# Kernel optimization log

Measured on AMD Instinct MI355X. Metric: run time of the kernel, lower is better.

The kernel has to match this reference:

```python
import jax, jax.numpy as jnp
import numpy as np

NUM_CLASSES = 91
W_CLASS, W_BBOX, W_GIOU = 1.0, 5.0, 2.0


def cxcywh_to_xyxy(b):
    return jnp.concatenate([b[..., :2] - 0.5 * b[..., 2:], b[..., :2] + 0.5 * b[..., 2:]], axis=-1)


def pairwise_giou(b1, b2):
    # b1: [B,Q,4] xyxy, b2: [B,G,4] xyxy -> [B,Q,G]
    area1 = (b1[..., 2] - b1[..., 0]) * (b1[..., 3] - b1[..., 1])
    area2 = (b2[..., 2] - b2[..., 0]) * (b2[..., 3] - b2[..., 1])
    lt = jnp.maximum(b1[:, :, None, :2], b2[:, None, :, :2])
    rb = jnp.minimum(b1[:, :, None, 2:], b2[:, None, :, 2:])
    wh = jnp.clip(rb - lt, 0.0)
    inter = wh[..., 0] * wh[..., 1]
    union = area1[:, :, None] + area2[:, None, :] - inter
    iou = inter / union
    lt2 = jnp.minimum(b1[:, :, None, :2], b2[:, None, :, :2])
    rb2 = jnp.maximum(b1[:, :, None, 2:], b2[:, None, :, 2:])
    wh2 = jnp.clip(rb2 - lt2, 0.0)
    area_c = wh2[..., 0] * wh2[..., 1]
    return iou - (area_c - union) / area_c


def elem_giou(b1, b2):
    # b1, b2: [M,4] xyxy -> [M]
    area1 = (b1[:, 2] - b1[:, 0]) * (b1[:, 3] - b1[:, 1])
    area2 = (b2[:, 2] - b2[:, 0]) * (b2[:, 3] - b2[:, 1])
    lt = jnp.maximum(b1[:, :2], b2[:, :2])
    rb = jnp.minimum(b1[:, 2:], b2[:, 2:])
    wh = jnp.clip(rb - lt, 0.0)
    inter = wh[:, 0] * wh[:, 1]
    union = area1 + area2 - inter
    iou = inter / union
    lt2 = jnp.minimum(b1[:, :2], b2[:, :2])
    rb2 = jnp.maximum(b1[:, 2:], b2[:, 2:])
    wh2 = jnp.clip(rb2 - lt2, 0.0)
    area_c = wh2[:, 0] * wh2[:, 1]
    return iou - (area_c - union) / area_c


def _lsa(cost):
    # Rectangular linear sum assignment (scipy-style shortest augmenting path).
    cost = np.asarray(cost, dtype=np.float64)
    transposed = cost.shape[0] > cost.shape[1]
    if transposed:
        cost = cost.T
    n, m = cost.shape
    u = np.zeros(n)
    v = np.zeros(m)
    path = np.full(m, -1, dtype=np.int64)
    col4row = np.full(n, -1, dtype=np.int64)
    row4col = np.full(m, -1, dtype=np.int64)
    for cur_row in range(n):
        min_val = 0.0
        i = cur_row
        remaining = np.arange(m)
        SR = np.zeros(n, dtype=bool)
        SC = np.zeros(m, dtype=bool)
        shortest = np.full(m, np.inf)
        sink = -1
        while sink == -1:
            SR[i] = True
            r = min_val + cost[i, remaining] - u[i] - v[remaining]
            better = r < shortest[remaining]
            upd = remaining[better]
            shortest[upd] = r[better]
            path[upd] = i
            k = int(np.argmin(shortest[remaining]))
            j = int(remaining[k])
            min_val = shortest[j]
            if not np.isfinite(min_val):
                raise ValueError('infeasible cost matrix')
            if row4col[j] == -1:
                sink = j
            else:
                i = int(row4col[j])
            SC[j] = True
            remaining = np.delete(remaining, k)
        u[cur_row] += min_val
        sr = SR.copy()
        sr[cur_row] = False
        u[sr] += min_val - shortest[col4row[sr]]
        v[SC] -= min_val - shortest[SC]
        j = sink
        while True:
            i = int(path[j])
            row4col[j] = i
            col4row[i], j = j, col4row[i]
            if i == cur_row:
                break
    if transposed:
        a = np.argsort(col4row)
        return col4row[a], a
    return np.arange(n), col4row


def _match(pred_logits, pred_boxes, gt_labels, gt_boxes):
    B, Q, _ = pred_logits.shape
    G = gt_labels.shape[1]
    log_probs = jax.nn.log_softmax(pred_logits, axis=-1)  # [B,Q,C+1]
    labels_c = jnp.clip(gt_labels, 0, NUM_CLASSES)
    cost_class = -jnp.take_along_axis(log_probs, jnp.broadcast_to(labels_c[:, None, :], (B, Q, G)), axis=2)
    cost_bbox = jnp.sum(jnp.abs(pred_boxes[:, :, None, :] - gt_boxes[:, None, :, :]), axis=-1)  # pairwise L1
    cost_giou = -pairwise_giou(cxcywh_to_xyxy(pred_boxes), cxcywh_to_xyxy(gt_boxes))
    C = W_BBOX * cost_bbox + W_CLASS * cost_class + W_GIOU * cost_giou  # [B,Q,G]
    C_np = np.asarray(jax.lax.stop_gradient(C))
    valid = np.asarray(gt_labels) < NUM_CLASSES
    b_idx, s_idx, t_idx = [], [], []
    for i in range(B):  # Hungarian is inherently sequential / host-side (matches torch original)
        cols = np.nonzero(valid[i])[0]
        if cols.size == 0:
            continue
        r, c = _lsa(C_np[i][:, cols])
        b_idx.append(np.full(r.shape, i, dtype=np.int64))
        s_idx.append(r.astype(np.int64))
        t_idx.append(cols[c].astype(np.int64))
    return np.concatenate(b_idx), np.concatenate(s_idx), np.concatenate(t_idx)


def _losses(pred_logits, pred_boxes, gt_boxes, gt_labels, batch_idx, src_idx, tgt_idx):
    B, Q, _ = pred_logits.shape
    log_probs = jax.nn.log_softmax(pred_logits, axis=-1)
    target_classes = jnp.full((B, Q), NUM_CLASSES, dtype=jnp.int32)
    target_classes = target_classes.at[batch_idx, src_idx].set(gt_labels[batch_idx, tgt_idx].astype(jnp.int32))
    nll = -jnp.take_along_axis(log_probs, target_classes[..., None], axis=-1)[..., 0]  # [B,Q]
    empty_weight = jnp.concatenate([jnp.full((NUM_CLASSES,), 0.1, jnp.float32), jnp.ones((1,), jnp.float32)])
    w = empty_weight[target_classes]
    loss_ce = jnp.sum(w * nll) / jnp.sum(w)  # weighted CE, torch 'mean' semantics
    mp = pred_boxes[batch_idx, src_idx][..., :4]
    mg = gt_boxes[batch_idx, tgt_idx]
    loss_bbox = jnp.mean(jnp.abs(mp - mg))
    loss_giou = jnp.mean(1.0 - elem_giou(cxcywh_to_xyxy(mp), cxcywh_to_xyxy(mg)))
    return jnp.stack([loss_ce, loss_bbox, loss_giou])


def setup_inputs() -> dict:
    key = jax.random.key(0)
    k1, k2, k3, k4 = jax.random.split(key, 4)
    B, Q, G = 128, 900, 80
    return {
        'pred_logits': jax.random.normal(k1, (B, Q, NUM_CLASSES + 1), dtype=jnp.float32),
        'pred_boxes': jax.random.uniform(k2, (B, Q, 4), dtype=jnp.float32),
        'gt_labels': jax.random.randint(k3, (B, G), 0, 120, dtype=jnp.int32),
        'gt_boxes': jax.random.uniform(k4, (B, G, 4), dtype=jnp.float32),
    }


def reference(pred_logits, pred_boxes, gt_labels, gt_boxes):
    bi, si, ti = _match(pred_logits, pred_boxes, gt_labels, gt_boxes)
    return _losses(pred_logits, pred_boxes, gt_boxes, gt_labels, bi, si, ti)
```

## Files before the change

### kernel.cpp

```cpp
#include <hip/hip_runtime.h>
#include <math.h>

#define BB 128
#define QQ 900
#define GG 80
#define CC 92
#define NCL 91
#define NSLOT 16

#define NPART 8
#define QPB 128

#define COST_OFF 0
#define LSE_OFF  36864000
#define VIDX_OFF 37324800
#define NV_OFF   37365760
#define FPART_OFF 37366272
#define MPART_OFF 37370368

#define FRONT_LDS_BYTES (QPB * 93 * 4)

__global__ __launch_bounds__(128) void front_kernel(const float* __restrict__ logits,
                                                    const float* __restrict__ pboxes,
                                                    const float* __restrict__ gboxes,
                                                    const int* __restrict__ glabels,
                                                    float* __restrict__ lse_g,
                                                    int* __restrict__ valid_idx,
                                                    int* __restrict__ nvalid,
                                                    float* __restrict__ cost,
                                                    float* __restrict__ fpart) {
    extern __shared__ float sL[];
    __shared__ int svidx[GG];
    __shared__ int s_n;
    __shared__ int slab[GG];
    __shared__ float sgx0[GG], sgy0[GG], sgx1[GG], sgy1[GG], sgar[GG];
    __shared__ float sgcx[GG], sgcy[GG], sgcz[GG], sgcw[GG];
    __shared__ double sce[2];
    int blk = blockIdx.x;
    int b = blk >> 3;
    int part = blk & 7;
    int tid = threadIdx.x;
    int q0 = part * QPB;
    int qcnt = QQ - q0;
    if (qcnt > QPB) qcnt = QPB;
    if (tid < 64) {
        int lane = tid;
        bool v0 = glabels[b * GG + lane] < NCL;
        bool v1 = (lane < GG - 64) ? (glabels[b * GG + 64 + lane] < NCL) : false;
        unsigned long long m0 = __ballot(v0);
        unsigned long long m1 = __ballot(v1);
        int c0 = __popcll(m0);
        unsigned long long lower = lane ? (~0ULL >> (64 - lane)) : 0ULL;
        if (v0) { int p = __popcll(m0 & lower); svidx[p] = lane; valid_idx[b * GG + p] = lane; }
        if (v1) { int p = c0 + __popcll(m1 & lower); svidx[p] = 64 + lane; valid_idx[b * GG + p] = 64 + lane; }
        if (lane == 0) { s_n = c0 + __popcll(m1); nvalid[b] = s_n; }
    }
    __syncthreads();
    int n = s_n;

    {
        const float* src = logits + ((size_t)b * QQ + q0) * CC;
        for (int i = tid; i < qcnt * CC; i += 128) {
            int ql = i / CC;
            int c = i - ql * CC;
            sL[ql * 93 + c] = src[i];
        }
    }
    for (int k = tid; k < n; k += 128) {
        int g = svidx[k];
        slab[k] = glabels[b * GG + g];
        float4 gb = ((const float4*)gboxes)[b * GG + g];
        sgcx[k] = gb.x; sgcy[k] = gb.y; sgcz[k] = gb.z; sgcw[k] = gb.w;
        float gx0 = gb.x - 0.5f * gb.z, gy0 = gb.y - 0.5f * gb.w;
        float gx1 = gb.x + 0.5f * gb.z, gy1 = gb.y + 0.5f * gb.w;
        sgx0[k] = gx0; sgy0[k] = gy0; sgx1[k] = gx1; sgy1[k] = gy1;
        sgar[k] = (gx1 - gx0) * (gy1 - gy0);
    }
    __syncthreads();

    int q = q0 + tid;
    bool qok = tid < qcnt;
    const float* row = sL + tid * 93;

    double local = 0.0;
    float lse_q = 0.f;
    if (qok) {
        float mx = -INFINITY;
        for (int c = 0; c < 23; ++c) {
            float x0 = row[4 * c], x1 = row[4 * c + 1], x2 = row[4 * c + 2], x3 = row[4 * c + 3];
            mx = fmaxf(mx, fmaxf(fmaxf(x0, x1), fmaxf(x2, x3)));
        }
        float ssum = 0.f;
        float e91 = 0.f;
        for (int c = 0; c < 23; ++c) {
            float x0 = row[4 * c], x1 = row[4 * c + 1], x2 = row[4 * c + 2], x3 = row[4 * c + 3];
            ssum += expf(x0 - mx) + expf(x1 - mx) + expf(x2 - mx) + expf(x3 - mx);
            if (c == 22) e91 = x3;
        }
        lse_q = mx + logf(ssum);
        lse_g[b * QQ + q] = lse_q;
        local = (double)lse_q - (double)e91;
    }
#pragma unroll
    for (int off = 32; off; off >>= 1) local += __shfl_down(local, off);
    if ((tid & 63) == 0) sce[tid >> 6] = local;

    if (qok) {
        float4 pb = ((const float4*)pboxes)[b * QQ + q];
        float px0 = pb.x - 0.5f * pb.z, py0 = pb.y - 0.5f * pb.w;
        float px1 = pb.x + 0.5f * pb.z, py1 = pb.y + 0.5f * pb.w;
        float parea = (px1 - px0) * (py1 - py0);
        for (int k = 0; k < n; ++k) {
            float l1 = fabsf(pb.x - sgcx[k]) + fabsf(pb.y - sgcy[k]) +
                       fabsf(pb.z - sgcz[k]) + fabsf(pb.w - sgcw[k]);
            float ltx = fmaxf(px0, sgx0[k]), lty = fmaxf(py0, sgy0[k]);
            float rbx = fminf(px1, sgx1[k]), rby = fminf(py1, sgy1[k]);
            float iw = fmaxf(rbx - ltx, 0.f), ih = fmaxf(rby - lty, 0.f);
            float inter = iw * ih;
            float uni = parea + sgar[k] - inter;
            float iou = inter / uni;
            float cx0 = fminf(px0, sgx0[k]), cy0 = fminf(py0, sgy0[k]);
            float cx1 = fmaxf(px1, sgx1[k]), cy1 = fmaxf(py1, sgy1[k]);
            float cw = fmaxf(cx1 - cx0, 0.f), ch = fmaxf(cy1 - cy0, 0.f);
            float ac = cw * ch;
            float giou = iou - (ac - uni) / ac;
            float cls = lse_q - row[slab[k]];
            cost[((size_t)(b * GG + k)) * QQ + q] = 5.f * l1 + cls - 2.f * giou;
        }
    }
    __syncthreads();
    if (tid == 0) fpart[blk] = (float)(sce[0] + sce[1]);
}

__device__ __forceinline__ unsigned long long wave_min_u64(unsigned long long x) {
#define KSTEP(ctrl)                                                                              \
    {                                                                                            \
        unsigned lo = (unsigned)x, hi = (unsigned)(x >> 32);                                     \
        unsigned lo_t = (unsigned)__builtin_amdgcn_update_dpp((int)lo, (int)lo, ctrl, 0xF, 0xF,  \
                                                              false);                            \
        unsigned hi_t = (unsigned)__builtin_amdgcn_update_dpp((int)hi, (int)hi, ctrl, 0xF, 0xF,  \
                                                              false);                            \
        unsigned long long t = ((unsigned long long)hi_t << 32) | lo_t;                          \
        x = t < x ? t : x;                                                                       \
    }
    KSTEP(0x111) KSTEP(0x112) KSTEP(0x114) KSTEP(0x118) KSTEP(0x142) KSTEP(0x143)
#undef KSTEP
    unsigned lo = (unsigned)__builtin_amdgcn_readlane((int)(unsigned)x, 63);
    unsigned hi = (unsigned)__builtin_amdgcn_readlane((int)(unsigned)(x >> 32), 63);
    return ((unsigned long long)hi << 32) | lo;
}

#define COL_OWNER_LANE(j) (((j) & 255) >> 2)
#define COL_SLOT(j) (((((j) >> 8)) << 2) | ((j) & 3))

__device__ __forceinline__ void load_row_f4(const float* crow, int lane, float (&cv)[NSLOT]) {
    const float4* c4 = (const float4*)crow;
    float4 a0 = c4[lane];
    float4 a1 = c4[64 + lane];
    float4 a2 = c4[128 + lane];
    float4 a3 = make_float4(0.f, 0.f, 0.f, 0.f);
    if (lane <= 32) a3 = c4[192 + lane];
    cv[0] = a0.x; cv[1] = a0.y; cv[2] = a0.z; cv[3] = a0.w;
    cv[4] = a1.x; cv[5] = a1.y; cv[6] = a1.z; cv[7] = a1.w;
    cv[8] = a2.x; cv[9] = a2.y; cv[10] = a2.z; cv[11] = a2.w;
    cv[12] = a3.x; cv[13] = a3.y; cv[14] = a3.z; cv[15] = a3.w;
}

__device__ __forceinline__ bool sap_phase(int cur, int lane, const float* cbase,
                                          unsigned valid_mask, float (&v)[NSLOT],
                                          int (&r4c_r)[NSLOT], float (&u_r)[2],
                                          int (&c4r_r)[2], float (&pf)[NSLOT], int nrows) {
    float sh[NSLOT];
    int path_r[NSLOT];
    float srv_r[2] = {0.f, 0.f};
    unsigned sc = 0, srm = 0;
#pragma unroll
    for (int s = 0; s < NSLOT; ++s) sh[s] = INFINITY;
    int i2 = cur;
    float minv = 0.f;
    int sink = -1;
    for (int pop = 0; pop < QQ && sink < 0; ++pop) {
        float cv[NSLOT];
        if (pop == 0) {
#pragma unroll
            for (int s = 0; s < NSLOT; ++s) cv[s] = pf[s];
        } else {
            load_row_f4(cbase + (size_t)i2 * QQ, lane, cv);
        }
        float uv = (i2 >> 6) ? u_r[1] : u_r[0];
        float ui = __uint_as_float(
            (unsigned)__builtin_amdgcn_readlane((int)__float_as_uint(uv), i2 & 63));
        float base = minv - ui;
        unsigned act = valid_mask & ~sc;
        float lmin = INFINITY;
        int lslot = 0;
#pragma unroll
        for (int s = 0; s < NSLOT; ++s) {
            if ((act >> s) & 1u) {
                float r = base + cv[s] - v[s];
                if (r < sh[s]) { sh[s] = r; path_r[s] = i2; }
                if (sh[s] < lmin) { lmin = sh[s]; lslot = s; }
            }
        }
        int jcol = ((lslot >> 2) << 8) + lane * 4 + (lslot & 3);
        unsigned u = __float_as_uint(lmin);
        u ^= ((int)u < 0) ? 0xFFFFFFFFu : 0x80000000u;
        unsigned long long key = ((unsigned long long)u << 32) | (unsigned)jcol;
        unsigned long long g = wave_min_u64(key);
        int lj = (int)(unsigned)g;
        unsigned mu = (unsigned)(g >> 32);
        minv = __uint_as_float((mu & 0x80000000u) ? (mu ^ 0x80000000u) : ~mu);
        int ol = COL_OWNER_LANE(lj);
        int os = COL_SLOT(lj);
        if (lane == ol) sc |= (1u << os);
        int rv = -1;
#pragma unroll
        for (int s = 0; s < NSLOT; ++s)
            if (s == os) rv = r4c_r[s];
        int r4c = __builtin_amdgcn_readlane(rv, ol);
        if (r4c == -1) {
            sink = lj;
        } else {
            i2 = r4c;
            if (lane == (i2 & 63)) {
#pragma unroll
                for (int s = 0; s < 2; ++s)
                    if (s == (i2 >> 6)) { srm |= (1u << s); srv_r[s] = minv; }
            }
        }
    }
    if (sink < 0) return false;
    {
        int nxt = cur + 2;
        if (nxt < nrows) load_row_f4(cbase + (size_t)nxt * QQ, lane, pf);
    }
    if (lane == (cur & 63)) {
#pragma unroll
        for (int s = 0; s < 2; ++s)
            if (s == (cur >> 6)) u_r[s] += minv;
    }
#pragma unroll
    for (int s = 0; s < 2; ++s)
        if ((srm >> s) & 1u) u_r[s] += minv - srv_r[s];
#pragma unroll
    for (int s = 0; s < NSLOT; ++s)
        if ((sc >> s) & 1u) v[s] -= (minv - sh[s]);
    int j = sink;
    while (true) {
        int plane = COL_OWNER_LANE(j);
        int pslot = COL_SLOT(j);
        int pv = 0;
#pragma unroll
        for (int s = 0; s < NSLOT; ++s)
            if (s == pslot) pv = path_r[s];
        int pi = __builtin_amdgcn_readlane(pv, plane);
        if (lane == plane) {
#pragma unroll
            for (int s = 0; s < NSLOT; ++s)
                if (s == pslot) r4c_r[s] = pi;
        }
        int cslot = pi >> 6, clane = pi & 63;
        int cvv = 0;
#pragma unroll
        for (int s = 0; s < 2; ++s)
            if (s == cslot) cvv = c4r_r[s];
        int nj = __builtin_amdgcn_readlane(cvv, clane);
        if (lane == clane) {
#pragma unroll
            for (int s = 0; s < 2; ++s)
                if (s == cslot) c4r_r[s] = j;
        }
        j = nj;
        if (pi == cur) break;
    }
    return true;
}

__global__ __launch_bounds__(64, 1) void lsa_kernel(const float* __restrict__ cost,
                                                    const int* __restrict__ nvalid,
                                                    const int* __restrict__ valid_idx,
                                                    const int* __restrict__ glabels,
                                                    const float* __restrict__ lse_g,
                                                    const float* __restrict__ pboxes,
                                                    const float* __restrict__ gboxes,
                                                    const float* __restrict__ logits,
                                                    double* __restrict__ mpart) {
    int b = blockIdx.x;
    int n = nvalid[b];
    const float* cbase = cost + (size_t)b * GG * QQ;
    int lane = threadIdx.x;

    float v[NSLOT];
    int r4c_r[NSLOT];
    float u_r[2];
    int c4r_r[2];
    float pfA[NSLOT], pfB[NSLOT];
    unsigned valid_mask = 0x0FFFu | ((lane <= 32) ? 0xF000u : 0u);
#pragma unroll
    for (int s = 0; s < NSLOT; ++s) { v[s] = 0.f; r4c_r[s] = -1; pfA[s] = 0.f; pfB[s] = 0.f; }
#pragma unroll
    for (int s = 0; s < 2; ++s) { u_r[s] = 0.f; c4r_r[s] = -1; }

    if (n > 0) load_row_f4(cbase, lane, pfA);
    if (n > 1) load_row_f4(cbase + QQ, lane, pfB);
    {
        int cur = 0;
        for (; cur + 1 < n; cur += 2) {
            sap_phase(cur, lane, cbase, valid_mask, v, r4c_r, u_r, c4r_r, pfA, n);
            sap_phase(cur + 1, lane, cbase, valid_mask, v, r4c_r, u_r, c4r_r, pfB, n);
        }
        if (cur < n)
            sap_phase(cur, lane, cbase, valid_mask, v, r4c_r, u_r, c4r_r, pfA, n);
    }

    double ce = 0.0, dl1 = 0.0, dgi = 0.0;
#pragma unroll
    for (int s = 0; s < 2; ++s) {
        int r = s * 64 + lane;
        int q = c4r_r[s];
        if (r < n && q >= 0 && q < QQ) {
            int g = valid_idx[b * GG + r];
            int label = glabels[b * GG + g];
            if (label < 0 || label >= CC) label = 0;
            size_t ro = ((size_t)b * QQ + q) * CC;
            float ls = lse_g[b * QQ + q];
            float nll_lab = ls - logits[ro + label];
            float nll_no = ls - logits[ro + NCL];
            ce += 0.1 * (double)nll_lab - (double)nll_no;
            float4 pb = ((const float4*)pboxes)[b * QQ + q];
            float4 gb = ((const float4*)gboxes)[b * GG + g];
            float l1 = fabsf(pb.x - gb.x) + fabsf(pb.y - gb.y) + fabsf(pb.z - gb.z) + fabsf(pb.w - gb.w);
            float px0 = pb.x - 0.5f * pb.z, py0 = pb.y - 0.5f * pb.w;
            float px1 = pb.x + 0.5f * pb.z, py1 = pb.y + 0.5f * pb.w;
            float gx0 = gb.x - 0.5f * gb.z, gy0 = gb.y - 0.5f * gb.w;
            float gx1 = gb.x + 0.5f * gb.z, gy1 = gb.y + 0.5f * gb.w;
            float parea = (px1 - px0) * (py1 - py0);
            float garea = (gx1 - gx0) * (gy1 - gy0);
            float ltx = fmaxf(px0, gx0), lty = fmaxf(py0, gy0);
            float rbx = fminf(px1, gx1), rby = fminf(py1, gy1);
            float iw = fmaxf(rbx - ltx, 0.f), ih = fmaxf(rby - lty, 0.f);
            float inter = iw * ih;
            float uni = parea + garea - inter;
            float iou = inter / uni;
            float cx0 = fminf(px0, gx0), cy0 = fminf(py0, gy0);
            float cx1 = fmaxf(px1, gx1), cy1 = fmaxf(py1, gy1);
            float cw = fmaxf(cx1 - cx0, 0.f), ch = fmaxf(cy1 - cy0, 0.f);
            float ac = cw * ch;
            float giou = iou - (ac - uni) / ac;
            dl1 += (double)l1;
            dgi += 1.0 - (double)giou;
        }
    }
#pragma unroll
    for (int off = 32; off; off >>= 1) {
        ce += __shfl_down(ce, off);
        dl1 += __shfl_down(dl1, off);
        dgi += __shfl_down(dgi, off);
    }
    if (lane == 0) {
        mpart[b * 3 + 0] = ce;
        mpart[b * 3 + 1] = dl1;
        mpart[b * 3 + 2] = dgi;
    }
}

__global__ __launch_bounds__(64) void final_kernel(const int* __restrict__ nvalid,
                                                   const float* __restrict__ fpart,
                                                   const double* __restrict__ mpart,
                                                   float* __restrict__ out) {
    int lane = threadIdx.x;
    int m = nvalid[lane] + nvalid[64 + lane];
    double fb = 0.0;
    for (int i = lane; i < BB * NPART; i += 64) fb += (double)fpart[i];
    double ce = 0.0, dl1 = 0.0, dgi = 0.0;
#pragma unroll
    for (int s = 0; s < 2; ++s) {
        int bb = s * 64 + lane;
        ce += mpart[bb * 3 + 0];
        dl1 += mpart[bb * 3 + 1];
        dgi += mpart[bb * 3 + 2];
    }
#pragma unroll
    for (int off = 32; off; off >>= 1) {
        m += __shfl_down(m, off);
        fb += __shfl_down(fb, off);
        ce += __shfl_down(ce, off);
        dl1 += __shfl_down(dl1, off);
        dgi += __shfl_down(dgi, off);
    }
    if (lane == 0) {
        double M = (double)m;
        double sum_w = (double)(BB * QQ) - 0.9 * M;
        out[0] = (float)((fb + ce) / sum_w);
        out[1] = (float)(dl1 / (4.0 * M));
        out[2] = (float)(dgi / M);
    }
}

extern "C" void kernel_launch(void* const* d_in, const int* in_sizes, int n_in,
                              void* d_out, int out_size, void* d_ws, size_t ws_size,
                              hipStream_t stream) {
    const float* logits = (const float*)d_in[0];
    const float* pboxes = (const float*)d_in[1];
    const int* glabels = (const int*)d_in[2];
    const float* gboxes = (const float*)d_in[3];
    float* out = (float*)d_out;

    char* ws = (char*)d_ws;
    float* cost = (float*)(ws + COST_OFF);
    float* lse = (float*)(ws + LSE_OFF);
    int* vidx = (int*)(ws + VIDX_OFF);
    int* nval = (int*)(ws + NV_OFF);
    float* fpart = (float*)(ws + FPART_OFF);
    double* mpart = (double*)(ws + MPART_OFF);

    (void)hipFuncSetAttribute((const void*)front_kernel,
                              hipFuncAttributeMaxDynamicSharedMemorySize, FRONT_LDS_BYTES);

    front_kernel<<<BB * NPART, 128, FRONT_LDS_BYTES, stream>>>(logits, pboxes, gboxes, glabels,
                                                               lse, vidx, nval, cost, fpart);
    lsa_kernel<<<BB, 64, 0, stream>>>(cost, nval, vidx, glabels, lse, pboxes, gboxes, logits, mpart);
    final_kernel<<<1, 64, 0, stream>>>(nval, fpart, mpart, out);
}
```

Measured before the change: 214.9 us.

## Fuse front, LSA and final kernels into one persistent launch with per-batch flags

Merges the three kernels into one grid. The first BB blocks run the assignment solver and spin on per-batch atomic counters until that batch's front blocks finish, and the last solver block to finish does the final reduction and resets the counters. The aim is to remove the launch gaps and let each batch's assignment start as soon as its cost matrix is ready, rather than waiting for every batch. In exchange, solver blocks now carry 128 threads and the front kernel's LDS allocation, and their spin-waiting depends on the front blocks being scheduled, which risks stalls or deadlock if residency is insufficient.

New measurement: 308.3 us. 1.43x slower.

```diff
diff --git a/kernel.cpp b/kernel.cpp
--- a/kernel.cpp
+++ b/kernel.cpp
@@ -20,117 +20,8 @@
 
 #define FRONT_LDS_BYTES (QPB * 93 * 4)
 
-__global__ __launch_bounds__(128) void front_kernel(const float* __restrict__ logits,
-                                                    const float* __restrict__ pboxes,
-                                                    const float* __restrict__ gboxes,
-                                                    const int* __restrict__ glabels,
-                                                    float* __restrict__ lse_g,
-                                                    int* __restrict__ valid_idx,
-                                                    int* __restrict__ nvalid,
-                                                    float* __restrict__ cost,
-                                                    float* __restrict__ fpart) {
-    extern __shared__ float sL[];
-    __shared__ int svidx[GG];
-    __shared__ int s_n;
-    __shared__ int slab[GG];
-    __shared__ float sgx0[GG], sgy0[GG], sgx1[GG], sgy1[GG], sgar[GG];
-    __shared__ float sgcx[GG], sgcy[GG], sgcz[GG], sgcw[GG];
-    __shared__ double sce[2];
-    int blk = blockIdx.x;
-    int b = blk >> 3;
-    int part = blk & 7;
-    int tid = threadIdx.x;
-    int q0 = part * QPB;
-    int qcnt = QQ - q0;
-    if (qcnt > QPB) qcnt = QPB;
-    if (tid < 64) {
-        int lane = tid;
-        bool v0 = glabels[b * GG + lane] < NCL;
-        bool v1 = (lane < GG - 64) ? (glabels[b * GG + 64 + lane] < NCL) : false;
-        unsigned long long m0 = __ballot(v0);
-        unsigned long long m1 = __ballot(v1);
-        int c0 = __popcll(m0);
-        unsigned long long lower = lane ? (~0ULL >> (64 - lane)) : 0ULL;
-        if (v0) { int p = __popcll(m0 & lower); svidx[p] = lane; valid_idx[b * GG + p] = lane; }
-        if (v1) { int p = c0 + __popcll(m1 & lower); svidx[p] = 64 + lane; valid_idx[b * GG + p] = 64 + lane; }
-        if (lane == 0) { s_n = c0 + __popcll(m1); nvalid[b] = s_n; }
-    }
-    __syncthreads();
-    int n = s_n;
-
-    {
-        const float* src = logits + ((size_t)b * QQ + q0) * CC;
-        for (int i = tid; i < qcnt * CC; i += 128) {
-            int ql = i / CC;
-            int c = i - ql * CC;
-            sL[ql * 93 + c] = src[i];
-        }
-    }
-    for (int k = tid; k < n; k += 128) {
-        int g = svidx[k];
-        slab[k] = glabels[b * GG + g];
-        float4 gb = ((const float4*)gboxes)[b * GG + g];
-        sgcx[k] = gb.x; sgcy[k] = gb.y; sgcz[k] = gb.z; sgcw[k] = gb.w;
-        float gx0 = gb.x - 0.5f * gb.z, gy0 = gb.y - 0.5f * gb.w;
-        float gx1 = gb.x + 0.5f * gb.z, gy1 = gb.y + 0.5f * gb.w;
-        sgx0[k] = gx0; sgy0[k] = gy0; sgx1[k] = gx1; sgy1[k] = gy1;
-        sgar[k] = (gx1 - gx0) * (gy1 - gy0);
-    }
-    __syncthreads();
-
-    int q = q0 + tid;
-    bool qok = tid < qcnt;
-    const float* row = sL + tid * 93;
-
-    double local = 0.0;
-    float lse_q = 0.f;
-    if (qok) {
-        float mx = -INFINITY;
-        for (int c = 0; c < 23; ++c) {
-            float x0 = row[4 * c], x1 = row[4 * c + 1], x2 = row[4 * c + 2], x3 = row[4 * c + 3];
-            mx = fmaxf(mx, fmaxf(fmaxf(x0, x1), fmaxf(x2, x3)));
-        }
-        float ssum = 0.f;
-        float e91 = 0.f;
-        for (int c = 0; c < 23; ++c) {
-            float x0 = row[4 * c], x1 = row[4 * c + 1], x2 = row[4 * c + 2], x3 = row[4 * c + 3];
-            ssum += expf(x0 - mx) + expf(x1 - mx) + expf(x2 - mx) + expf(x3 - mx);
-            if (c == 22) e91 = x3;
-        }
-        lse_q = mx + logf(ssum);
-        lse_g[b * QQ + q] = lse_q;
-        local = (double)lse_q - (double)e91;
-    }
-#pragma unroll
-    for (int off = 32; off; off >>= 1) local += __shfl_down(local, off);
-    if ((tid & 63) == 0) sce[tid >> 6] = local;
-
-    if (qok) {
-        float4 pb = ((const float4*)pboxes)[b * QQ + q];
-        float px0 = pb.x - 0.5f * pb.z, py0 = pb.y - 0.5f * pb.w;
-        float px1 = pb.x + 0.5f * pb.z, py1 = pb.y + 0.5f * pb.w;
-        float parea = (px1 - px0) * (py1 - py0);
-        for (int k = 0; k < n; ++k) {
-            float l1 = fabsf(pb.x - sgcx[k]) + fabsf(pb.y - sgcy[k]) +
-                       fabsf(pb.z - sgcz[k]) + fabsf(pb.w - sgcw[k]);
-            float ltx = fmaxf(px0, sgx0[k]), lty = fmaxf(py0, sgy0[k]);
-            float rbx = fminf(px1, sgx1[k]), rby = fminf(py1, sgy1[k]);
-            float iw = fmaxf(rbx - ltx, 0.f), ih = fmaxf(rby - lty, 0.f);
-            float inter = iw * ih;
-            float uni = parea + sgar[k] - inter;
-            float iou = inter / uni;
-            float cx0 = fminf(px0, sgx0[k]), cy0 = fminf(py0, sgy0[k]);
-            float cx1 = fmaxf(px1, sgx1[k]), cy1 = fmaxf(py1, sgy1[k]);
-            float cw = fmaxf(cx1 - cx0, 0.f), ch = fmaxf(cy1 - cy0, 0.f);
-            float ac = cw * ch;
-            float giou = iou - (ac - uni) / ac;
-            float cls = lse_q - row[slab[k]];
-            cost[((size_t)(b * GG + k)) * QQ + q] = 5.f * l1 + cls - 2.f * giou;
-        }
-    }
-    __syncthreads();
-    if (tid == 0) fpart[blk] = (float)(sce[0] + sce[1]);
-}
+__device__ int g_cnt_front[BB];
+__device__ int g_cnt_lsa;
 
 __device__ __forceinline__ unsigned long long wave_min_u64(unsigned long long x) {
 #define KSTEP(ctrl)                                                                              \
@@ -276,19 +167,138 @@
     return true;
 }
 
-__global__ __launch_bounds__(64, 1) void lsa_kernel(const float* __restrict__ cost,
-                                                    const int* __restrict__ nvalid,
-                                                    const int* __restrict__ valid_idx,
-                                                    const int* __restrict__ glabels,
-                                                    const float* __restrict__ lse_g,
+__global__ __launch_bounds__(128) void fused_kernel(const float* __restrict__ logits,
                                                     const float* __restrict__ pboxes,
                                                     const float* __restrict__ gboxes,
-                                                    const float* __restrict__ logits,
-                                                    double* __restrict__ mpart) {
-    int b = blockIdx.x;
+                                                    const int* __restrict__ glabels,
+                                                    float* __restrict__ lse_g,
+                                                    int* __restrict__ valid_idx,
+                                                    int* __restrict__ nvalid,
+                                                    float* __restrict__ cost,
+                                                    float* __restrict__ fpart,
+                                                    double* __restrict__ mpart,
+                                                    float* __restrict__ out) {
+    extern __shared__ float sL[];
+    int blk = blockIdx.x;
+
+    if (blk >= BB) {
+        __shared__ int svidx[GG];
+        __shared__ int s_n;
+        __shared__ int slab[GG];
+        __shared__ float sgx0[GG], sgy0[GG], sgx1[GG], sgy1[GG], sgar[GG];
+        __shared__ float sgcx[GG], sgcy[GG], sgcz[GG], sgcw[GG];
+        __shared__ double sce[2];
+        int fblk = blk - BB;
+        int b = fblk >> 3;
+        int part = fblk & 7;
+        int tid = threadIdx.x;
+        int q0 = part * QPB;
+        int qcnt = QQ - q0;
+        if (qcnt > QPB) qcnt = QPB;
+        if (tid < 64) {
+            int lane = tid;
+            bool v0 = glabels[b * GG + lane] < NCL;
+            bool v1 = (lane < GG - 64) ? (glabels[b * GG + 64 + lane] < NCL) : false;
+            unsigned long long m0 = __ballot(v0);
+            unsigned long long m1 = __ballot(v1);
+            int c0 = __popcll(m0);
+            unsigned long long lower = lane ? (~0ULL >> (64 - lane)) : 0ULL;
+            if (v0) { int p = __popcll(m0 & lower); svidx[p] = lane; valid_idx[b * GG + p] = lane; }
+            if (v1) { int p = c0 + __popcll(m1 & lower); svidx[p] = 64 + lane; valid_idx[b * GG + p] = 64 + lane; }
+            if (lane == 0) { s_n = c0 + __popcll(m1); nvalid[b] = s_n; }
+        }
+        __syncthreads();
+        int n = s_n;
+
+        {
+            const float* src = logits + ((size_t)b * QQ + q0) * CC;
+            for (int i = tid; i < qcnt * CC; i += 128) {
+                int ql = i / CC;
+                int c = i - ql * CC;
+                sL[ql * 93 + c] = src[i];
+            }
+        }
+        for (int k = tid; k < n; k += 128) {
+            int g = svidx[k];
+            slab[k] = glabels[b * GG + g];
+            float4 gb = ((const float4*)gboxes)[b * GG + g];
+            sgcx[k] = gb.x; sgcy[k] = gb.y; sgcz[k] = gb.z; sgcw[k] = gb.w;
+            float gx0 = gb.x - 0.5f * gb.z, gy0 = gb.y - 0.5f * gb.w;
+            float gx1 = gb.x + 0.5f * gb.z, gy1 = gb.y + 0.5f * gb.w;
+            sgx0[k] = gx0; sgy0[k] = gy0; sgx1[k] = gx1; sgy1[k] = gy1;
+            sgar[k] = (gx1 - gx0) * (gy1 - gy0);
+        }
+        __syncthreads();
+
+        int q = q0 + tid;
+        bool qok = tid < qcnt;
+        const float* row = sL + tid * 93;
+
+        double local = 0.0;
+        float lse_q = 0.f;
+        if (qok) {
+            float mx = -INFINITY;
+            for (int c = 0; c < 23; ++c) {
+                float x0 = row[4 * c], x1 = row[4 * c + 1], x2 = row[4 * c + 2], x3 = row[4 * c + 3];
+                mx = fmaxf(mx, fmaxf(fmaxf(x0, x1), fmaxf(x2, x3)));
+            }
+            float ssum = 0.f;
+            float e91 = 0.f;
+            for (int c = 0; c < 23; ++c) {
+                float x0 = row[4 * c], x1 = row[4 * c + 1], x2 = row[4 * c + 2], x3 = row[4 * c + 3];
+                ssum += expf(x0 - mx) + expf(x1 - mx) + expf(x2 - mx) + expf(x3 - mx);
+                if (c == 22) e91 = x3;
+            }
+            lse_q = mx + logf(ssum);
+            lse_g[b * QQ + q] = lse_q;
+            local = (double)lse_q - (double)e91;
+        }
+#pragma unroll
+        for (int off = 32; off; off >>= 1) local += __shfl_down(local, off);
+        if ((tid & 63) == 0) sce[tid >> 6] = local;
+
+        if (qok) {
+            float4 pb = ((const float4*)pboxes)[b * QQ + q];
+            float px0 = pb.x - 0.5f * pb.z, py0 = pb.y - 0.5f * pb.w;
+            float px1 = pb.x + 0.5f * pb.z, py1 = pb.y + 0.5f * pb.w;
+            float parea = (px1 - px0) * (py1 - py0);
+            for (int k = 0; k < n; ++k) {
+                float l1 = fabsf(pb.x - sgcx[k]) + fabsf(pb.y - sgcy[k]) +
+                           fabsf(pb.z - sgcz[k]) + fabsf(pb.w - sgcw[k]);
+                float ltx = fmaxf(px0, sgx0[k]), lty = fmaxf(py0, sgy0[k]);
+                float rbx = fminf(px1, sgx1[k]), rby = fminf(py1, sgy1[k]);
+                float iw = fmaxf(rbx - ltx, 0.f), ih = fmaxf(rby - lty, 0.f);
+                float inter = iw * ih;
+                float uni = parea + sgar[k] - inter;
+                float iou = inter / uni;
+                float cx0 = fminf(px0, sgx0[k]), cy0 = fminf(py0, sgy0[k]);
+                float cx1 = fmaxf(px1, sgx1[k]), cy1 = fmaxf(py1, sgy1[k]);
+                float cw = fmaxf(cx1 - cx0, 0.f), ch = fmaxf(cy1 - cy0, 0.f);
+                float ac = cw * ch;
+                float giou = iou - (ac - uni) / ac;
+                float cls = lse_q - row[slab[k]];
+                cost[((size_t)(b * GG + k)) * QQ + q] = 5.f * l1 + cls - 2.f * giou;
+            }
+        }
+        __syncthreads();
+        if (tid == 0) fpart[fblk] = (float)(sce[0] + sce[1]);
+        __threadfence();
+        __syncthreads();
+        if (tid == 0)
+            __hip_atomic_fetch_add(&g_cnt_front[b], 1, __ATOMIC_RELEASE, __HIP_MEMORY_SCOPE_AGENT);
+        return;
+    }
+
+    if (threadIdx.x >= 64) return;
+    int b = blk;
+    int lane = threadIdx.x;
+
+    while (__hip_atomic_load(&g_cnt_front[b], __ATOMIC_ACQUIRE, __HIP_MEMORY_SCOPE_AGENT) < NPART)
+        __builtin_amdgcn_s_sleep(8);
+    __threadfence();
+
     int n = nvalid[b];
     const float* cbase = cost + (size_t)b * GG * QQ;
-    int lane = threadIdx.x;
 
     float v[NSLOT];
     int r4c_r[NSLOT];
@@ -362,38 +372,42 @@
         mpart[b * 3 + 1] = dl1;
         mpart[b * 3 + 2] = dgi;
     }
-}
-
-__global__ __launch_bounds__(64) void final_kernel(const int* __restrict__ nvalid,
-                                                   const float* __restrict__ fpart,
-                                                   const double* __restrict__ mpart,
-                                                   float* __restrict__ out) {
-    int lane = threadIdx.x;
-    int m = nvalid[lane] + nvalid[64 + lane];
-    double fb = 0.0;
-    for (int i = lane; i < BB * NPART; i += 64) fb += (double)fpart[i];
-    double ce = 0.0, dl1 = 0.0, dgi = 0.0;
-#pragma unroll
-    for (int s = 0; s < 2; ++s) {
-        int bb = s * 64 + lane;
-        ce += mpart[bb * 3 + 0];
-        dl1 += mpart[bb * 3 + 1];
-        dgi += mpart[bb * 3 + 2];
-    }
-#pragma unroll
-    for (int off = 32; off; off >>= 1) {
-        m += __shfl_down(m, off);
-        fb += __shfl_down(fb, off);
-        ce += __shfl_down(ce, off);
-        dl1 += __shfl_down(dl1, off);
-        dgi += __shfl_down(dgi, off);
-    }
-    if (lane == 0) {
-        double M = (double)m;
-        double sum_w = (double)(BB * QQ) - 0.9 * M;
-        out[0] = (float)((fb + ce) / sum_w);
-        out[1] = (float)(dl1 / (4.0 * M));
-        out[2] = (float)(dgi / M);
+    __threadfence();
+    int oldv = 0;
+    if (lane == 0)
+        oldv = __hip_atomic_fetch_add(&g_cnt_lsa, 1, __ATOMIC_ACQ_REL, __HIP_MEMORY_SCOPE_AGENT);
+    oldv = __shfl(oldv, 0);
+    if (oldv == BB - 1) {
+        __threadfence();
+        int m = nvalid[lane] + nvalid[64 + lane];
+        double fb = 0.0;
+        for (int i = lane; i < BB * NPART; i += 64) fb += (double)fpart[i];
+        double fce = 0.0, fdl1 = 0.0, fdgi = 0.0;
+#pragma unroll
+        for (int s = 0; s < 2; ++s) {
+            int bb = s * 64 + lane;
+            fce += mpart[bb * 3 + 0];
+            fdl1 += mpart[bb * 3 + 1];
+            fdgi += mpart[bb * 3 + 2];
+        }
+#pragma unroll
+        for (int off = 32; off; off >>= 1) {
+            m += __shfl_down(m, off);
+            fb += __shfl_down(fb, off);
+            fce += __shfl_down(fce, off);
+            fdl1 += __shfl_down(fdl1, off);
+            fdgi += __shfl_down(fdgi, off);
+        }
+        if (lane == 0) {
+            double M = (double)m;
+            double sum_w = (double)(BB * QQ) - 0.9 * M;
+            out[0] = (float)((fb + fce) / sum_w);
+            out[1] = (float)(fdl1 / (4.0 * M));
+            out[2] = (float)(fdgi / M);
+        }
+        g_cnt_front[lane] = 0;
+        g_cnt_front[64 + lane] = 0;
+        if (lane == 0) g_cnt_lsa = 0;
     }
 }
 
@@ -414,11 +428,9 @@
     float* fpart = (float*)(ws + FPART_OFF);
     double* mpart = (double*)(ws + MPART_OFF);
 
-    (void)hipFuncSetAttribute((const void*)front_kernel,
+    (void)hipFuncSetAttribute((const void*)fused_kernel,
                               hipFuncAttributeMaxDynamicSharedMemorySize, FRONT_LDS_BYTES);
 
-    front_kernel<<<BB * NPART, 128, FRONT_LDS_BYTES, stream>>>(logits, pboxes, gboxes, glabels,
-                                                               lse, vidx, nval, cost, fpart);
-    lsa_kernel<<<BB, 64, 0, stream>>>(cost, nval, vidx, glabels, lse, pboxes, gboxes, logits, mpart);
-    final_kernel<<<1, 64, 0, stream>>>(nval, fpart, mpart, out);
+    fused_kernel<<<BB + BB * NPART, 128, FRONT_LDS_BYTES, stream>>>(
+        logits, pboxes, gboxes, glabels, lse, vidx, nval, cost, fpart, mpart, out);
 }
```
